# Performance work log

Measured on AMD Instinct MI355X. Metric: run time of the kernel, lower is better.

## Reference

```python
import jax, jax.numpy as jnp
import numpy as np

E = 1024   # embed_dim
H = 16     # num_heads
D = E // H # head_dim = 64
HD2 = D // 2
B = 2
S = 2048


def setup_inputs() -> dict:
    key = jax.random.key(0)
    ks = jax.random.split(key, 12)
    def lin(k, fan_in, fan_out):
        # xavier-uniform-ish init, stored in [in, out] (jax) convention
        lim = float(np.sqrt(6.0 / (fan_in + fan_out)))
        return jax.random.uniform(k, (fan_in, fan_out), jnp.float32, -lim, lim)
    return {
        "query": jax.random.normal(ks[0], (B, S, E), jnp.float32),
        "xi_scale": jax.random.uniform(ks[1], (B,), jnp.float32),
        "Wq": lin(ks[2], E, E), "bq": jnp.zeros((E,), jnp.float32),
        "Wk": lin(ks[3], E, E), "bk": jnp.zeros((E,), jnp.float32),
        "Wv": lin(ks[4], E, E), "bv": jnp.zeros((E,), jnp.float32),
        "Wo": lin(ks[5], E, E), "bo": jnp.zeros((E,), jnp.float32),
        "enc_w1": lin(ks[6], 1, HD2), "enc_b1": jnp.zeros((HD2,), jnp.float32),
        "ln_g": jnp.ones((HD2,), jnp.float32), "ln_b": jnp.zeros((HD2,), jnp.float32),
        "enc_w2": lin(ks[7], HD2, D), "enc_b2": jnp.zeros((D,), jnp.float32),
        "scale_gating": jnp.ones((H,), jnp.float32),
    }


def reference(query, xi_scale, Wq, bq, Wk, bk, Wv, bv, Wo, bo,
              enc_w1, enc_b1, ln_g, ln_b, enc_w2, enc_b2, scale_gating):
    b, s, e = query.shape
    h, d = H, e // H
    # --- scale adaptation: xi -> Linear -> LayerNorm -> GELU -> Linear ---
    x = xi_scale[:, None] @ enc_w1 + enc_b1                  # [B, D/2]
    mu = x.mean(-1, keepdims=True)
    var = ((x - mu) ** 2).mean(-1, keepdims=True)
    x = (x - mu) / jnp.sqrt(var + 1e-5) * ln_g + ln_b
    x = jax.nn.gelu(x, approximate=False)
    xe = x @ enc_w2 + enc_b2                                 # [B, D]
    adapt = 1.0 + jax.nn.sigmoid(scale_gating)[None, :, None] * xe[:, None, :]  # [B, H, D]
    # --- projections (self-attention: key = value = query) ---
    q = (query @ Wq + bq).reshape(b, s, h, d).transpose(0, 2, 1, 3) * adapt[:, :, None, :]
    k = (query @ Wk + bk).reshape(b, s, h, d).transpose(0, 2, 1, 3) * adapt[:, :, None, :]
    v = (query @ Wv + bv).reshape(b, s, h, d).transpose(0, 2, 1, 3)
    # --- explicit QK^T / sqrt(d) -> softmax -> V ---
    inv_scale = 1.0 / float(np.sqrt(d))
    scores = jnp.einsum('bhqd,bhkd->bhqk', q, k) * inv_scale  # [B, H, S, S]
    attn = jax.nn.softmax(scores, axis=-1)
    out = jnp.einsum('bhqk,bhkd->bhqd', attn, v)              # [B, H, S, D]
    out = out.transpose(0, 2, 1, 3).reshape(b, s, e)
    return out @ Wo + bo
```

## Files before the change

### kernel.cpp

```cpp
#include <hip/hip_runtime.h>

typedef __bf16 bf16;
typedef __attribute__((ext_vector_type(8))) __bf16 bf16x8;
typedef __attribute__((ext_vector_type(4))) float f32x4;
typedef __attribute__((ext_vector_type(16))) float f32x16;
typedef unsigned int u32;

#define MFMA16(a, b, c) __builtin_amdgcn_mfma_f32_16x16x32_bf16((a), (b), (c), 0, 0, 0)
#define MFMA32(a, b, c) __builtin_amdgcn_mfma_f32_32x32x16_bf16((a), (b), (c), 0, 0, 0)

#define BB 2
#define SS 2048
#define EE 1024
#define HH 16
#define DD 64
#define MM (BB * SS)
#define NT (SS / 64)

__device__ inline f32x4 zero4() {
    f32x4 z; z.x = 0.f; z.y = 0.f; z.z = 0.f; z.w = 0.f; return z;
}

__device__ __forceinline__ void gload16(const bf16* g, bf16* l) {
    __builtin_amdgcn_global_load_lds(
        (const __attribute__((address_space(1))) u32*)(const void*)g,
        (__attribute__((address_space(3))) u32*)(void*)l,
        16, 0, 0);
}

__device__ __forceinline__ u32 pkbf(float a, float b) {
    union { __bf16 h; unsigned short s; } ua, ub;
    ua.h = (__bf16)a; ub.h = (__bf16)b;
    return (u32)ua.s | ((u32)ub.s << 16);
}

__global__ __launch_bounds__(256) void prep_kernel(
    const float* __restrict__ query, bf16* __restrict__ qc,
    const float* __restrict__ s0, const float* __restrict__ s1,
    const float* __restrict__ s2, const float* __restrict__ s3,
    bf16* __restrict__ d0, bf16* __restrict__ d1,
    bf16* __restrict__ d2, bf16* __restrict__ d3,
    const float* __restrict__ xi, const float* __restrict__ w1,
    const float* __restrict__ b1, const float* __restrict__ lng,
    const float* __restrict__ lnb, const float* __restrict__ w2,
    const float* __restrict__ b2, const float* __restrict__ gate,
    float* __restrict__ adapt) {
    __shared__ bf16 tile[64 * 72];
    const int bid = blockIdx.x;
    const int t = threadIdx.x;

    if (bid < 2048) {
        const int i = (bid * 256 + t) * 8;
        float4 a = *(const float4*)(query + i);
        float4 b = *(const float4*)(query + i + 4);
        bf16 tmp[8];
        tmp[0] = (bf16)a.x; tmp[1] = (bf16)a.y; tmp[2] = (bf16)a.z; tmp[3] = (bf16)a.w;
        tmp[4] = (bf16)b.x; tmp[5] = (bf16)b.y; tmp[6] = (bf16)b.z; tmp[7] = (bf16)b.w;
        *(uint4*)(qc + i) = *(uint4*)tmp;
    } else if (bid < 3072) {
        const int m = (bid - 2048) >> 8;
        const int idx0 = (bid - 2048) & 255;
        const float* W = (m == 0) ? s0 : (m == 1) ? s1 : (m == 2) ? s2 : s3;
        bf16* Wt = (m == 0) ? d0 : (m == 1) ? d1 : (m == 2) ? d2 : d3;
        const int k0 = (idx0 >> 4) * 64, n0 = (idx0 & 15) * 64;
#pragma unroll
        for (int i = 0; i < 2; ++i) {
            int idx = i * 256 + t;
            int r = idx >> 3, c = (idx & 7) * 8;
            float4 a = *(const float4*)(W + (k0 + r) * EE + n0 + c);
            float4 b = *(const float4*)(W + (k0 + r) * EE + n0 + c + 4);
            bf16 tmp[8];
            tmp[0] = (bf16)a.x; tmp[1] = (bf16)a.y; tmp[2] = (bf16)a.z; tmp[3] = (bf16)a.w;
            tmp[4] = (bf16)b.x; tmp[5] = (bf16)b.y; tmp[6] = (bf16)b.z; tmp[7] = (bf16)b.w;
            *(uint4*)(tile + r * 72 + c) = *(uint4*)tmp;
        }
        __syncthreads();
#pragma unroll
        for (int i = 0; i < 2; ++i) {
            int idx = i * 256 + t;
            int n = idx >> 3, kc = (idx & 7) * 8;
            bf16 tmp[8];
#pragma unroll
            for (int j = 0; j < 8; ++j) tmp[j] = tile[(kc + j) * 72 + n];
            *(uint4*)(Wt + (n0 + n) * EE + k0 + kc) = *(uint4*)tmp;
        }
    } else {
        const int b = bid - 3072;
        float* xs = (float*)tile;
        if (t < 64) {
            const float xiv = xi[b];
            float xv = 0.f;
            if (t < 32) xv = xiv * w1[t] + b1[t];
            float sm = xv;
            for (int off = 1; off < 32; off <<= 1) sm += __shfl_xor(sm, off);
            const float mu = sm * (1.f / 32.f);
            float dv = (t < 32) ? (xv - mu) : 0.f;
            float s2 = dv * dv;
            for (int off = 1; off < 32; off <<= 1) s2 += __shfl_xor(s2, off);
            const float var = s2 * (1.f / 32.f);
            if (t < 32) {
                float xn = (xv - mu) * rsqrtf(var + 1e-5f) * lng[t] + lnb[t];
                float ge = 0.5f * xn * (1.f + erff(xn * 0.70710678118654752f));
                xs[t] = ge;
            }
        }
        __syncthreads();
        if (t < 64) {
            float acc = b2[t];
            for (int j = 0; j < 32; ++j) acc += xs[j] * w2[j * DD + t];
            for (int h = 0; h < HH; ++h) {
                float sg = 1.f / (1.f + __expf(-gate[h]));
                adapt[(b * HH + h) * DD + t] = 1.f + sg * acc;
            }
        }
    }
}

__global__ __launch_bounds__(256, 3) void gemm_qkv(
    const bf16* __restrict__ Aq, const bf16* __restrict__ Bqk,
    const bf16* __restrict__ Av,
    const float* __restrict__ bias, const float* __restrict__ bias2,
    const float* __restrict__ bias3, const float* __restrict__ adapt,
    bf16* __restrict__ outqk, bf16* __restrict__ outvt) {
    __shared__ bf16 sh[16384];
    bf16* As = sh;
    bf16* Bs = sh + 8192;

    const int t = threadIdx.x;
    const int w = t >> 6, lane = t & 63;
    const int mrow = lane & 15, quad = lane >> 4;
    const int wm = (w & 1) * 64, wn = (w >> 1) * 64;

    int md, bx, by;
    const bf16 *Ap, *Bp;
    int bid = blockIdx.x;
    if (bid < 512) { md = 5; bx = bid & 31; by = bid >> 5; Ap = Aq; Bp = Bqk; }
    else { md = 4; bid -= 512; bx = bid & 7; by = bid >> 3; Ap = Av; Bp = Aq; }
    const int m0 = bx * 128, n0 = by * 128;
    const int m2 = (md == 5) ? (by >> 3) : 0;

    f32x4 acc[4][4];
#pragma unroll
    for (int i = 0; i < 4; ++i)
#pragma unroll
        for (int j = 0; j < 4; ++j) acc[i][j] = zero4();

    const int dr = lane >> 2;
    const int dcg = ((lane & 3) ^ (dr & 3)) * 8;
    const bf16* Ag = Ap + (size_t)(m0 + w * 16 + dr) * EE + dcg;
    const bf16* Bg = Bp + (size_t)(n0 + w * 16 + dr) * EE + dcg;
    bf16* Al = As + (w * 16) * 32;
    bf16* Bl = Bs + (w * 16) * 32;

    gload16(Ag, Al);
    gload16(Ag + 64 * EE, Al + 64 * 32);
    gload16(Bg, Bl);
    gload16(Bg + 64 * EE, Bl + 64 * 32);

    for (int kt = 0; kt < 32; ++kt) {
        __syncthreads();
        if (kt < 31) {
            const int kn = (kt + 1) * 32;
            const int nb = (kt + 1) & 1;
            gload16(Ag + kn, Al + nb * 4096);
            gload16(Ag + 64 * EE + kn, Al + nb * 4096 + 64 * 32);
            gload16(Bg + kn, Bl + nb * 4096);
            gload16(Bg + 64 * EE + kn, Bl + nb * 4096 + 64 * 32);
        }
        const bf16* Ab = As + (kt & 1) * 4096;
        const bf16* Bb = Bs + (kt & 1) * 4096;
        const int sw = (quad ^ (mrow & 3)) * 8;
        bf16x8 af[4], bfr[4];
#pragma unroll
        for (int i = 0; i < 4; ++i)
            af[i] = *(const bf16x8*)(Ab + (wm + i * 16 + mrow) * 32 + sw);
#pragma unroll
        for (int j = 0; j < 4; ++j)
            bfr[j] = *(const bf16x8*)(Bb + (wn + j * 16 + mrow) * 32 + sw);
#pragma unroll
        for (int i = 0; i < 4; ++i)
#pragma unroll
            for (int j = 0; j < 4; ++j)
                acc[i][j] = MFMA16(af[i], bfr[j], acc[i][j]);
    }

    __syncthreads();

    if (md == 5) {
        const int bq_ = m0 >> 11;
        float cmul[4], cadd[4];
#pragma unroll
        for (int j = 0; j < 4; ++j) {
            const int cl = (n0 & 1023) + wn + j * 16 + mrow;
            const int hh = cl >> 6, dd2 = cl & 63;
            const float ad = adapt[(bq_ * HH + hh) * DD + dd2];
            const float sc = m2 ? 1.f : 0.18033688011113811f;
            cmul[j] = ad * sc;
            cadd[j] = (m2 ? bias2[cl] : bias[cl]) * ad * sc;
        }
#pragma unroll
        for (int i = 0; i < 4; ++i)
#pragma unroll
            for (int j = 0; j < 4; ++j) {
                const int lcol = wn + j * 16 + mrow;
#pragma unroll
                for (int r = 0; r < 4; ++r) {
                    const int lrow = wm + i * 16 + quad * 4 + r;
                    const float v = acc[i][j][r] * cmul[j] + cadd[j];
                    *(bf16*)((char*)sh + lrow * 256 +
                             ((lcol * 2) ^ ((lrow & 15) << 4))) = (bf16)v;
                }
            }
    } else {
        float radd[16];
#pragma unroll
        for (int i = 0; i < 4; ++i)
#pragma unroll
            for (int r = 0; r < 4; ++r)
                radd[i * 4 + r] = bias3[m0 + wm + i * 16 + quad * 4 + r];
#pragma unroll
        for (int i = 0; i < 4; ++i)
#pragma unroll
            for (int j = 0; j < 4; ++j) {
                const int lcol = wn + j * 16 + mrow;
#pragma unroll
                for (int r = 0; r < 4; ++r) {
                    const int lrow = wm + i * 16 + quad * 4 + r;
                    const float v = acc[i][j][r] + radd[i * 4 + r];
                    *(bf16*)((char*)sh + lrow * 256 +
                             ((lcol * 2) ^ ((lrow & 15) << 4))) = (bf16)v;
                }
            }
    }
    __syncthreads();

#pragma unroll
    for (int p = 0; p < 8; ++p) {
        const int lrow = p * 16 + (t >> 4);
        const int lcol0 = (t & 15) * 8;
        bf16x8 val = *(const bf16x8*)((const char*)sh + lrow * 256 +
                                      ((lcol0 * 2) ^ ((lrow & 15) << 4)));
        if (md == 5) {
            const int bq_ = m0 >> 11;
            const int s_ = (m0 + lrow) & (SS - 1);
            const int cl = (n0 & 1023) + lcol0;
            const int hh = cl >> 6, d0 = cl & 63;
            if (!m2) {
                *(bf16x8*)(outqk + ((size_t)(bq_ * HH + hh) * SS + s_) * DD + d0) = val;
            } else {
                const size_t base = (size_t)MM * EE + (size_t)(bq_ * HH + hh) * 131072;
                const int a2 = (s_ >> 6) * 4096 + ((s_ >> 5) & 1) * 2048 +
                               (d0 >> 4) * 512 +
                               ((s_ & 31) + ((d0 >> 3) & 1) * 32) * 8;
                *(bf16x8*)(outqk + base + a2) = val;
            }
        } else {
            const int rowv = m0 + lrow;
            const int hv = rowv >> 6, dv = rowv & 63;
            const int colv = n0 + lcol0;
            const int bv_ = colv >> 11, sv = colv & (SS - 1);
            const size_t base = (size_t)(bv_ * HH + hv) * 131072;
            const int a2 = (sv >> 6) * 4096 + (dv >> 5) * 2048 +
                           ((sv >> 4) & 3) * 512 +
                           ((dv & 31) + ((sv >> 3) & 1) * 32) * 8;
            *(bf16x8*)(outvt + base + a2) = val;
        }
    }
}

__global__ __launch_bounds__(256, 3) void gemm_o(
    const bf16* __restrict__ A, const bf16* __restrict__ Bt,
    const float* __restrict__ bias, float* __restrict__ outf) {
    __shared__ bf16 As[2 * 128 * 64];
    __shared__ bf16 Bs[2 * 64 * 64];

    const int t = threadIdx.x;
    const int w = t >> 6, lane = t & 63;
    const int mrow = lane & 15, quad = lane >> 4;
    const int m0 = blockIdx.x * 128, n0 = blockIdx.y * 64;

    f32x4 acc[2][4];
#pragma unroll
    for (int i = 0; i < 2; ++i)
#pragma unroll
        for (int j = 0; j < 4; ++j) acc[i][j] = zero4();

    const int grow = lane >> 3;
    const int gsw = ((lane & 7) ^ grow) * 8;
    const bf16* Ag = A + (size_t)(m0 + w * 32 + grow) * EE + gsw;
    const bf16* Bg = Bt + (size_t)(n0 + w * 16 + grow) * EE + gsw;
    bf16* Al = As + (w * 32) * 64;
    bf16* Bl = Bs + (w * 16) * 64;

#pragma unroll
    for (int i = 0; i < 4; ++i) gload16(Ag + i * 8 * EE, Al + i * 8 * 64);
#pragma unroll
    for (int i = 0; i < 2; ++i) gload16(Bg + i * 8 * EE, Bl + i * 8 * 64);

    for (int kt = 0; kt < 16; ++kt) {
        __syncthreads();
        if (kt < 15) {
            const int kn = (kt + 1) * 64;
            const int nb = (kt + 1) & 1;
#pragma unroll
            for (int i = 0; i < 4; ++i)
                gload16(Ag + i * 8 * EE + kn, Al + nb * 8192 + i * 8 * 64);
#pragma unroll
            for (int i = 0; i < 2; ++i)
                gload16(Bg + i * 8 * EE + kn, Bl + nb * 4096 + i * 8 * 64);
        }
        const bf16* Ab = As + (kt & 1) * 8192;
        const bf16* Bb = Bs + (kt & 1) * 4096;
#pragma unroll
        for (int ks = 0; ks < 2; ++ks) {
            const int cg = ks * 4 + quad;
            const int sw = (cg ^ (mrow & 7)) * 8;
            bf16x8 af[2], bfr[4];
#pragma unroll
            for (int mi = 0; mi < 2; ++mi)
                af[mi] = *(const bf16x8*)(Ab + (w * 32 + mi * 16 + mrow) * 64 + sw);
#pragma unroll
            for (int nj = 0; nj < 4; ++nj)
                bfr[nj] = *(const bf16x8*)(Bb + (nj * 16 + mrow) * 64 + sw);
#pragma unroll
            for (int mi = 0; mi < 2; ++mi)
#pragma unroll
                for (int nj = 0; nj < 4; ++nj)
                    acc[mi][nj] = MFMA16(af[mi], bfr[nj], acc[mi][nj]);
        }
    }

    __syncthreads();
    char* fs = (char*)As;
    float cadd[4];
#pragma unroll
    for (int nj = 0; nj < 4; ++nj) cadd[nj] = bias[n0 + nj * 16 + mrow];
#pragma unroll
    for (int mi = 0; mi < 2; ++mi)
#pragma unroll
        for (int nj = 0; nj < 4; ++nj) {
            const int lcol = nj * 16 + mrow;
#pragma unroll
            for (int r = 0; r < 4; ++r) {
                const int lrow = w * 32 + mi * 16 + quad * 4 + r;
                *(float*)(fs + lrow * 256 + ((lcol * 4) ^ ((lrow & 15) << 4))) =
                    acc[mi][nj][r] + cadd[nj];
            }
        }
    __syncthreads();

#pragma unroll
    for (int p = 0; p < 8; ++p) {
        const int lrow = p * 16 + (t >> 4);
        const int lcol0 = (t & 15) * 4;
        float4 val = *(const float4*)(fs + lrow * 256 +
                                      ((lcol0 * 4) ^ ((lrow & 15) << 4)));
        *(float4*)(outf + (size_t)(m0 + lrow) * EE + n0 + lcol0) = val;
    }
}

__device__ __forceinline__ void attn_step(
    int kt, const bf16* kbase, const bf16* vbase,
    const bf16x8 (&qf)[4], bf16x8 (&KU)[8], bf16x8 (&KP)[8],
    f32x16 (&oacc)[2], float (&ls)[4], int h) {
    __builtin_amdgcn_s_barrier();

    bf16x8 vf[8];
#pragma unroll
    for (int mf = 0; mf < 2; ++mf)
#pragma unroll
        for (int c = 0; c < 4; ++c)
            vf[mf * 4 + c] = *(const bf16x8*)(vbase + kt * 4096 + mf * 2048 + c * 512);

    f32x16 st[2];
#pragma unroll
    for (int mf = 0; mf < 2; ++mf)
#pragma unroll
        for (int i = 0; i < 16; ++i) st[mf][i] = 0.f;
    __builtin_amdgcn_s_setprio(1);
#pragma unroll
    for (int c = 0; c < 4; ++c)
#pragma unroll
        for (int mf = 0; mf < 2; ++mf)
            st[mf] = MFMA32(KU[mf * 4 + c], qf[c], st[mf]);
    __builtin_amdgcn_s_setprio(0);

    const int ktp = kt + (kt < NT - 1 ? 1 : 0);
#pragma unroll
    for (int mf = 0; mf < 2; ++mf)
#pragma unroll
        for (int c = 0; c < 4; ++c)
            KP[mf * 4 + c] = *(const bf16x8*)(kbase + ktp * 4096 + mf * 2048 + c * 512);

    u32 P32[2][8];
#pragma unroll
    for (int mf = 0; mf < 2; ++mf)
#pragma unroll
        for (int rp = 0; rp < 8; ++rp) {
            float pa = __builtin_amdgcn_exp2f(st[mf][2 * rp]);
            float pb = __builtin_amdgcn_exp2f(st[mf][2 * rp + 1]);
            ls[rp & 3] += pa + pb;
            P32[mf][rp] = pkbf(pa, pb);
        }

#pragma unroll
    for (int c = 0; c < 4; ++c) {
        const int mfs = c >> 1;
        const int ro = (c & 1) * 4;
        union { u32 u[4]; bf16x8 v; } pb;
        {
            u32 vA0 = P32[mfs][ro + 0], vA1 = P32[mfs][ro + 1];
            u32 vB0 = P32[mfs][ro + 2], vB1 = P32[mfs][ro + 3];
            u32 prep0 = h ? vA0 : vB0;
            u32 prep1 = h ? vA1 : vB1;
            u32 sh0 = __shfl_xor(prep0, 32);
            u32 sh1 = __shfl_xor(prep1, 32);
            pb.u[0] = h ? sh0 : vA0;
            pb.u[1] = h ? sh1 : vA1;
            pb.u[2] = h ? vB0 : sh0;
            pb.u[3] = h ? vB1 : sh1;
        }
        __builtin_amdgcn_s_setprio(1);
#pragma unroll
        for (int mf = 0; mf < 2; ++mf)
            oacc[mf] = MFMA32(vf[mf * 4 + c], pb.v, oacc[mf]);
        __builtin_amdgcn_s_setprio(0);
    }
}

__global__ __launch_bounds__(256, 2) void attn_kernel(
    const bf16* __restrict__ q, const bf16* __restrict__ k,
    const bf16* __restrict__ vt, bf16* __restrict__ o0) {
    __shared__ bf16 lds[4 * 2112];

    const int t = threadIdx.x;
    const int w = t >> 6, lane = t & 63;
    const int q32 = lane & 31, h = lane >> 5;
    const int bh = blockIdx.x & 31;
    const int qb = blockIdx.x >> 5;
    const int qr0 = qb * 128 + w * 32;

    bf16x8 qf[4];
#pragma unroll
    for (int c = 0; c < 4; ++c)
        qf[c] = *(const bf16x8*)(q + (size_t)(bh * SS + qr0 + q32) * DD + c * 16 + h * 8);

    const bf16* kbase = k + (size_t)bh * 131072 + lane * 8;
    const bf16* vbase = vt + (size_t)bh * 131072 + lane * 8;

    f32x16 oacc[2];
#pragma unroll
    for (int mf = 0; mf < 2; ++mf)
#pragma unroll
        for (int i = 0; i < 16; ++i) oacc[mf][i] = 0.f;
    float ls[4] = {0.f, 0.f, 0.f, 0.f};

    bf16x8 Ka[8], Kb[8];
#pragma unroll
    for (int mf = 0; mf < 2; ++mf)
#pragma unroll
        for (int c = 0; c < 4; ++c)
            Ka[mf * 4 + c] = *(const bf16x8*)(kbase + mf * 2048 + c * 512);

    for (int kt2 = 0; kt2 < NT / 2; ++kt2) {
        attn_step(2 * kt2,     kbase, vbase, qf, Ka, Kb, oacc, ls, h);
        attn_step(2 * kt2 + 1, kbase, vbase, qf, Kb, Ka, oacc, ls, h);
    }

    float lsum = (ls[0] + ls[1]) + (ls[2] + ls[3]);
    lsum += __shfl_xor(lsum, 32);
    const float inv = 1.f / lsum;

    bf16* ob = lds + w * 2112;
#pragma unroll
    for (int mf = 0; mf < 2; ++mf)
#pragma unroll
        for (int rp = 0; rp < 8; ++rp) {
            const int d = 32 * mf + 2 * (rp & 1) + 8 * (rp >> 1) + 4 * h;
            *(u32*)(ob + q32 * 66 + d) =
                pkbf(oacc[mf][2 * rp] * inv, oacc[mf][2 * rp + 1] * inv);
        }
    __syncthreads();

    const int b = bh >> 4, head = bh & 15;
    const int half = lane & 1;
    const int r = lane >> 1;
#pragma unroll
    for (int i = 0; i < 4; ++i) {
        bf16x8 val = *(const bf16x8*)(ob + r * 66 + half * 32 + i * 8);
        *(bf16x8*)(o0 + (size_t)(b * SS + qr0 + r) * EE + head * DD +
                   half * 32 + i * 8) = val;
    }
}

extern "C" void kernel_launch(void* const* d_in, const int* in_sizes, int n_in,
                              void* d_out, int out_size, void* d_ws, size_t ws_size,
                              hipStream_t stream) {
    const float* query = (const float*)d_in[0];
    const float* xi    = (const float*)d_in[1];
    const float* Wq = (const float*)d_in[2];  const float* bq = (const float*)d_in[3];
    const float* Wk = (const float*)d_in[4];  const float* bk = (const float*)d_in[5];
    const float* Wv = (const float*)d_in[6];  const float* bv = (const float*)d_in[7];
    const float* Wo = (const float*)d_in[8];  const float* bo = (const float*)d_in[9];
    const float* ew1 = (const float*)d_in[10]; const float* eb1 = (const float*)d_in[11];
    const float* lng = (const float*)d_in[12]; const float* lnb = (const float*)d_in[13];
    const float* ew2 = (const float*)d_in[14]; const float* eb2 = (const float*)d_in[15];
    const float* gate = (const float*)d_in[16];
    float* out = (float*)d_out;

    char* ws = (char*)d_ws;
    const size_t SZ = (size_t)MM * EE * sizeof(bf16);
    const size_t WSZ = (size_t)EE * EE * sizeof(bf16);

    bf16* queryc = (bf16*)(ws);
    bf16* p0     = (bf16*)(ws);
    bf16* qws    = (bf16*)(ws + SZ);
    bf16* kws    = (bf16*)(ws + 2 * SZ);
    bf16* vtws   = (bf16*)(ws + 3 * SZ);
    bf16* wqT    = (bf16*)(ws + 4 * SZ);
    bf16* wkT    = (bf16*)(ws + 4 * SZ + WSZ);
    bf16* wvT    = (bf16*)(ws + 4 * SZ + 2 * WSZ);
    bf16* woT    = (bf16*)(ws + 4 * SZ + 3 * WSZ);
    float* adaptws = (float*)(ws + 4 * SZ + 4 * WSZ);

    prep_kernel<<<3074, 256, 0, stream>>>(query, queryc, Wq, Wk, Wv, Wo,
                                          wqT, wkT, wvT, woT,
                                          xi, ew1, eb1, lng, lnb, ew2, eb2, gate,
                                          adaptws);

    gemm_qkv<<<768, 256, 0, stream>>>(queryc, wqT, wvT, bq, bk, bv, adaptws,
                                      qws, vtws);

    attn_kernel<<<512, 256, 0, stream>>>(qws, kws, vtws, p0);

    gemm_o<<<dim3(MM / 128, EE / 64), 256, 0, stream>>>(p0, woT, bo, out);
}
```

Before: 212.6 us.

## Software-pipeline attention loop: overlap QK of next tile with PV of previous

Restructures the attention inner loop so each step issues the QK^T MFMAs for tile T interleaved with the PV MFMAs for tile T-1, with the exp/pack for tile T done afterwards. This is meant to hide exp2 and pack latency behind matrix work. K is now prefetched two tiles ahead, V one tile ahead with double-buffered V and P registers. The cross-half P shuffle is replaced by v_permlane32_swap, and the per-step s_barrier is dropped. Register pressure rises substantially, which risks spills or lower occupancy under the 2-blocks launch bound.

```diff
diff --git a/kernel.cpp b/kernel.cpp
--- a/kernel.cpp
+++ b/kernel.cpp
@@ -33,6 +33,8 @@
     ua.h = (__bf16)a; ub.h = (__bf16)b;
     return (u32)ua.s | ((u32)ub.s << 16);
 }
+
+#define PSWAP(a, b) asm("v_permlane32_swap_b32 %0, %1" : "+v"(a), "+v"(b))
 
 __global__ __launch_bounds__(256) void prep_kernel(
     const float* __restrict__ query, bf16* __restrict__ qc,
@@ -359,74 +361,65 @@
     }
 }
 
-__device__ __forceinline__ void attn_step(
-    int kt, const bf16* kbase, const bf16* vbase,
-    const bf16x8 (&qf)[4], bf16x8 (&KU)[8], bf16x8 (&KP)[8],
-    f32x16 (&oacc)[2], float (&ls)[4], int h) {
-    __builtin_amdgcn_s_barrier();
-
-    bf16x8 vf[8];
-#pragma unroll
-    for (int mf = 0; mf < 2; ++mf)
-#pragma unroll
-        for (int c = 0; c < 4; ++c)
-            vf[mf * 4 + c] = *(const bf16x8*)(vbase + kt * 4096 + mf * 2048 + c * 512);
-
-    f32x16 st[2];
-#pragma unroll
-    for (int mf = 0; mf < 2; ++mf)
-#pragma unroll
-        for (int i = 0; i < 16; ++i) st[mf][i] = 0.f;
-    __builtin_amdgcn_s_setprio(1);
-#pragma unroll
-    for (int c = 0; c < 4; ++c)
-#pragma unroll
-        for (int mf = 0; mf < 2; ++mf)
-            st[mf] = MFMA32(KU[mf * 4 + c], qf[c], st[mf]);
-    __builtin_amdgcn_s_setprio(0);
-
-    const int ktp = kt + (kt < NT - 1 ? 1 : 0);
-#pragma unroll
-    for (int mf = 0; mf < 2; ++mf)
-#pragma unroll
-        for (int c = 0; c < 4; ++c)
-            KP[mf * 4 + c] = *(const bf16x8*)(kbase + ktp * 4096 + mf * 2048 + c * 512);
-
-    u32 P32[2][8];
-#pragma unroll
-    for (int mf = 0; mf < 2; ++mf)
-#pragma unroll
-        for (int rp = 0; rp < 8; ++rp) {
-            float pa = __builtin_amdgcn_exp2f(st[mf][2 * rp]);
-            float pb = __builtin_amdgcn_exp2f(st[mf][2 * rp + 1]);
-            ls[rp & 3] += pa + pb;
-            P32[mf][rp] = pkbf(pa, pb);
-        }
-
-#pragma unroll
-    for (int c = 0; c < 4; ++c) {
-        const int mfs = c >> 1;
-        const int ro = (c & 1) * 4;
-        union { u32 u[4]; bf16x8 v; } pb;
-        {
-            u32 vA0 = P32[mfs][ro + 0], vA1 = P32[mfs][ro + 1];
-            u32 vB0 = P32[mfs][ro + 2], vB1 = P32[mfs][ro + 3];
-            u32 prep0 = h ? vA0 : vB0;
-            u32 prep1 = h ? vA1 : vB1;
-            u32 sh0 = __shfl_xor(prep0, 32);
-            u32 sh1 = __shfl_xor(prep1, 32);
-            pb.u[0] = h ? sh0 : vA0;
-            pb.u[1] = h ? sh1 : vA1;
-            pb.u[2] = h ? vB0 : sh0;
-            pb.u[3] = h ? vB1 : sh1;
-        }
-        __builtin_amdgcn_s_setprio(1);
-#pragma unroll
-        for (int mf = 0; mf < 2; ++mf)
-            oacc[mf] = MFMA32(vf[mf * 4 + c], pb.v, oacc[mf]);
-        __builtin_amdgcn_s_setprio(0);
-    }
-}
+#define ATTN_SMPACK(ST0, ST1, PBN)                                           \
+    do {                                                                     \
+        u32 P32_[2][8];                                                      \
+        _Pragma("unroll")                                                    \
+        for (int rp = 0; rp < 8; ++rp) {                                     \
+            float pa_ = __builtin_amdgcn_exp2f((ST0)[2 * rp]);               \
+            float pb_ = __builtin_amdgcn_exp2f((ST0)[2 * rp + 1]);           \
+            ls[rp & 3] += pa_ + pb_;                                         \
+            P32_[0][rp] = pkbf(pa_, pb_);                                    \
+            float pc_ = __builtin_amdgcn_exp2f((ST1)[2 * rp]);               \
+            float pd_ = __builtin_amdgcn_exp2f((ST1)[2 * rp + 1]);           \
+            ls[rp & 3] += pc_ + pd_;                                         \
+            P32_[1][rp] = pkbf(pc_, pd_);                                    \
+        }                                                                    \
+        _Pragma("unroll")                                                    \
+        for (int c = 0; c < 4; ++c) {                                        \
+            const int mfs_ = c >> 1, ro_ = (c & 1) * 4;                      \
+            u32 a0_ = P32_[mfs_][ro_ + 0], a1_ = P32_[mfs_][ro_ + 1];        \
+            u32 b0_ = P32_[mfs_][ro_ + 2], b1_ = P32_[mfs_][ro_ + 3];        \
+            PSWAP(a0_, b0_); PSWAP(a1_, b1_);                                \
+            PBN[c * 4 + 0] = a0_; PBN[c * 4 + 1] = a1_;                      \
+            PBN[c * 4 + 2] = b0_; PBN[c * 4 + 3] = b1_;                      \
+        }                                                                    \
+    } while (0)
+
+#define ATTN_STEP(T, KU, VFP, VFN, PBP, PBN, DOPF)                           \
+    do {                                                                     \
+        _Pragma("unroll")                                                    \
+        for (int mf = 0; mf < 2; ++mf)                                       \
+            _Pragma("unroll")                                                \
+            for (int c = 0; c < 4; ++c)                                      \
+                VFN[mf * 4 + c] = *(const bf16x8*)(vbase + (T) * 4096 +      \
+                                                   mf * 2048 + c * 512);     \
+        f32x16 st0, st1;                                                     \
+        _Pragma("unroll")                                                    \
+        for (int i = 0; i < 16; ++i) { st0[i] = 0.f; st1[i] = 0.f; }         \
+        __builtin_amdgcn_s_setprio(1);                                       \
+        _Pragma("unroll")                                                    \
+        for (int c = 0; c < 4; ++c) {                                        \
+            st0 = MFMA32(KU[c], qf[c], st0);                                 \
+            st1 = MFMA32(KU[4 + c], qf[c], st1);                             \
+            union { u32 u[4]; bf16x8 v; } pv_;                               \
+            pv_.u[0] = PBP[c * 4 + 0]; pv_.u[1] = PBP[c * 4 + 1];            \
+            pv_.u[2] = PBP[c * 4 + 2]; pv_.u[3] = PBP[c * 4 + 3];            \
+            oacc[0] = MFMA32(VFP[c], pv_.v, oacc[0]);                        \
+            oacc[1] = MFMA32(VFP[4 + c], pv_.v, oacc[1]);                    \
+        }                                                                    \
+        __builtin_amdgcn_s_setprio(0);                                       \
+        if (DOPF) {                                                          \
+            const int ktp_ = ((T) + 2 < NT) ? (T) + 2 : NT - 1;              \
+            _Pragma("unroll")                                                \
+            for (int mf = 0; mf < 2; ++mf)                                   \
+                _Pragma("unroll")                                            \
+                for (int c = 0; c < 4; ++c)                                  \
+                    KU[mf * 4 + c] = *(const bf16x8*)(kbase + ktp_ * 4096 +  \
+                                                      mf * 2048 + c * 512);  \
+        }                                                                    \
+        ATTN_SMPACK(st0, st1, PBN);                                          \
+    } while (0)
 
 __global__ __launch_bounds__(256, 2) void attn_kernel(
     const bf16* __restrict__ q, const bf16* __restrict__ k,
@@ -450,22 +443,56 @@
 
     f32x16 oacc[2];
 #pragma unroll
+    for (int i = 0; i < 16; ++i) { oacc[0][i] = 0.f; oacc[1][i] = 0.f; }
+    float ls[4] = {0.f, 0.f, 0.f, 0.f};
+
+    bf16x8 Ka[8], Kb[8], vfA[8], vfB[8];
+    u32 pbA[16], pbB[16];
+
+#pragma unroll
     for (int mf = 0; mf < 2; ++mf)
 #pragma unroll
-        for (int i = 0; i < 16; ++i) oacc[mf][i] = 0.f;
-    float ls[4] = {0.f, 0.f, 0.f, 0.f};
-
-    bf16x8 Ka[8], Kb[8];
-#pragma unroll
-    for (int mf = 0; mf < 2; ++mf)
-#pragma unroll
-        for (int c = 0; c < 4; ++c)
+        for (int c = 0; c < 4; ++c) {
             Ka[mf * 4 + c] = *(const bf16x8*)(kbase + mf * 2048 + c * 512);
-
-    for (int kt2 = 0; kt2 < NT / 2; ++kt2) {
-        attn_step(2 * kt2,     kbase, vbase, qf, Ka, Kb, oacc, ls, h);
-        attn_step(2 * kt2 + 1, kbase, vbase, qf, Kb, Ka, oacc, ls, h);
-    }
+            Kb[mf * 4 + c] = *(const bf16x8*)(kbase + 4096 + mf * 2048 + c * 512);
+            vfA[mf * 4 + c] = *(const bf16x8*)(vbase + mf * 2048 + c * 512);
+        }
+
+    {
+        f32x16 st0, st1;
+#pragma unroll
+        for (int i = 0; i < 16; ++i) { st0[i] = 0.f; st1[i] = 0.f; }
+        __builtin_amdgcn_s_setprio(1);
+#pragma unroll
+        for (int c = 0; c < 4; ++c) {
+            st0 = MFMA32(Ka[c], qf[c], st0);
+            st1 = MFMA32(Ka[4 + c], qf[c], st1);
+        }
+        __builtin_amdgcn_s_setprio(0);
+#pragma unroll
+        for (int mf = 0; mf < 2; ++mf)
+#pragma unroll
+            for (int c = 0; c < 4; ++c)
+                Ka[mf * 4 + c] = *(const bf16x8*)(kbase + 2 * 4096 + mf * 2048 + c * 512);
+        ATTN_SMPACK(st0, st1, pbA);
+    }
+
+    for (int i = 0; i < 15; ++i) {
+        ATTN_STEP(2 * i + 1, Kb, vfA, vfB, pbA, pbB, 1);
+        ATTN_STEP(2 * i + 2, Ka, vfB, vfA, pbB, pbA, 1);
+    }
+    ATTN_STEP(31, Kb, vfA, vfB, pbA, pbB, 0);
+
+    __builtin_amdgcn_s_setprio(1);
+#pragma unroll
+    for (int c = 0; c < 4; ++c) {
+        union { u32 u[4]; bf16x8 v; } pv_;
+        pv_.u[0] = pbB[c * 4 + 0]; pv_.u[1] = pbB[c * 4 + 1];
+        pv_.u[2] = pbB[c * 4 + 2]; pv_.u[3] = pbB[c * 4 + 3];
+        oacc[0] = MFMA32(vfB[c], pv_.v, oacc[0]);
+        oacc[1] = MFMA32(vfB[4 + c], pv_.v, oacc[1]);
+    }
+    __builtin_amdgcn_s_setprio(0);
 
     float lsum = (ls[0] + ls[1]) + (ls[2] + ls[3]);
     lsum += __shfl_xor(lsum, 32);
```

New measurement: 206.7 us. 1.03x faster.
